# Performance work log

Measured on AMD Instinct MI355X. Metric: run time of the kernel, lower is better.

The kernel has to match this reference:

```python
import jax, jax.numpy as jnp
import numpy as np


def setup_inputs() -> dict:
    key = jax.random.key(0)
    k1, k2, k3 = jax.random.split(key, 3)
    B, D = 4096, 512
    out_ftir = jax.random.normal(k1, (B, D), dtype=jnp.float32)
    out_raman = jax.random.normal(k2, (B, D), dtype=jnp.float32)
    labels = jax.random.randint(k3, (B,), 0, 1000, dtype=jnp.int64)
    # learned parameter: log_tau = log(1/init_tau), init_tau = 0.07
    log_tau = jnp.asarray(np.log(1.0 / 0.07), dtype=jnp.float32)
    return {"out_ftir": out_ftir, "out_raman": out_raman, "labels": labels, "log_tau": log_tau}


def reference(out_ftir, out_raman, labels, log_tau):
    # temperature scale, clamped above at 100
    tau = jnp.minimum(jnp.exp(log_tau), 100.0)
    # [B, B] similarity logits
    logits = (out_ftir @ out_raman.T) * tau
    # CLIP-style symmetric cross-entropy with diagonal targets (arange(B)).
    # Note: original torch code's loop over positive off-diagonal pairs
    # computes an unused tensor and does not affect the output.
    raman_lp = jnp.diagonal(jax.nn.log_softmax(logits, axis=-1))   # rows: ftir -> raman
    ftir_lp = jnp.diagonal(jax.nn.log_softmax(logits.T, axis=-1))  # cols: raman -> ftir
    raman_loss = -jnp.mean(raman_lp)
    ftir_loss = -jnp.mean(ftir_lp)
    return (ftir_loss + raman_loss) / 2.0
```

## Files before the change

kernel.cpp:

```cpp
#include <hip/hip_runtime.h>
#include <hip/hip_bf16.h>
#include <stdint.h>


typedef float f32x4 __attribute__((ext_vector_type(4)));
typedef __bf16 bf16x8 __attribute__((ext_vector_type(8)));
typedef __bf16 bf16x4 __attribute__((ext_vector_type(4)));

#define B_DIM 4096
#define D_DIM 512
#define NCHUNK 32

__device__ __forceinline__ void gld_lds16(const void* g, void* l) {
  __builtin_amdgcn_global_load_lds(
      (const __attribute__((address_space(1))) unsigned int*)g,
      (__attribute__((address_space(3))) unsigned int*)l,
      16, 0, 0);
}

__global__ __launch_bounds__(256) void cast_diag_kernel(
    const float* __restrict__ A, const float* __restrict__ Bm,
    __bf16* __restrict__ Abf, __bf16* __restrict__ Bbf,
    float* __restrict__ diagp, float* __restrict__ acc,
    unsigned* __restrict__ counter) {
  if (blockIdx.x == 0 && threadIdx.x == 0) { acc[0] = 0.f; counter[0] = 0u; }
  const float4* A4 = (const float4*)A;
  const float4* B4 = (const float4*)Bm;
  bf16x4* Ab4 = (bf16x4*)Abf;
  bf16x4* Bb4 = (bf16x4*)Bbf;
  int idx = blockIdx.x * 256 + threadIdx.x;
  float local = 0.f;
  #pragma unroll
  for (int it = 0; it < 4; ++it, idx += 512 * 256) {
    int row = idx >> 7, el4 = idx & 127;
    int swzG = ((el4 >> 1) ^ row) & 7;
    int el4p = (el4 & 0x71) | (swzG << 1);
    int pidx = row * 128 + el4p;
    float4 va = A4[idx], vb = B4[idx];
    bf16x4 oa, ob;
    oa[0] = (__bf16)va.x; oa[1] = (__bf16)va.y; oa[2] = (__bf16)va.z; oa[3] = (__bf16)va.w;
    ob[0] = (__bf16)vb.x; ob[1] = (__bf16)vb.y; ob[2] = (__bf16)vb.z; ob[3] = (__bf16)vb.w;
    Ab4[pidx] = oa; Bb4[pidx] = ob;
    local += va.x*vb.x + va.y*vb.y + va.z*vb.z + va.w*vb.w;
  }
  #pragma unroll
  for (int off = 1; off < 64; off <<= 1) local += __shfl_xor(local, off);
  __shared__ float red[4];
  int w = threadIdx.x >> 6, lane = threadIdx.x & 63;
  if (lane == 0) red[w] = local;
  __syncthreads();
  if (threadIdx.x == 0)
    diagp[blockIdx.x] = red[0] + red[1] + red[2] + red[3];
}

__global__ __launch_bounds__(256) void gemm_lse_kernel(
    const __bf16* __restrict__ A, const __bf16* __restrict__ Bm,
    const float* __restrict__ log_tau,
    float* __restrict__ row_pmax, float* __restrict__ row_psum,
    float* __restrict__ col_pmax, float* __restrict__ col_psum) {
  __shared__ char smem[34816];
  __bf16* Alds = (__bf16*)smem;
  __bf16* Blds = (__bf16*)(smem + 16384);
  const int blk = blockIdx.x;
  const int xcd = blk & 7, local = blk >> 3;
  const int bm = (xcd & 3) * 8 + (local & 7);
  const int bn = (xcd >> 2) * 16 + (local >> 3);
  const int t = threadIdx.x;
  const int lane = t & 63;
  const int w = t >> 6;
  const int wm = (w >> 1) * 64, wn = (w & 1) * 64;
  const int q = lane >> 4, c16 = lane & 15, swz = c16 & 7;

  f32x4 acc[4][4] = {};

  const char* Ag = (const char*)(A + (size_t)(bm * 128 + (t >> 3)) * D_DIM + (t & 7) * 8);
  const char* Bg = (const char*)(Bm + (size_t)(bn * 128 + (t >> 3)) * D_DIM + (t & 7) * 8);
  char* Al = (char*)Alds + t * 16;
  char* Bl = (char*)Blds + t * 16;

  for (int kt = 0; kt < 8; ++kt) {
    const char* ag = Ag + kt * 128;
    const char* bg = Bg + kt * 128;
    #pragma unroll
    for (int i = 0; i < 4; ++i) {
      gld_lds16(ag + i * 32 * 1024, Al + i * 4096);
      gld_lds16(bg + i * 32 * 1024, Bl + i * 4096);
    }
    __syncthreads();
    const __bf16* Abase = Alds + (wm + c16) * 64;
    const __bf16* Bbase = Blds + (wn + c16) * 64;
    #pragma unroll
    for (int h = 0; h < 2; ++h) {
      const int kb = ((h << 2) | q) ^ swz;
      bf16x8 af[4], bfr[4];
      #pragma unroll
      for (int mi = 0; mi < 4; ++mi)
        af[mi] = *(const bf16x8*)(Abase + mi * 1024 + kb * 8);
      #pragma unroll
      for (int ni = 0; ni < 4; ++ni)
        bfr[ni] = *(const bf16x8*)(Bbase + ni * 1024 + kb * 8);
      #pragma unroll
      for (int mi = 0; mi < 4; ++mi)
        #pragma unroll
        for (int ni = 0; ni < 4; ++ni)
          acc[mi][ni] = __builtin_amdgcn_mfma_f32_16x16x32_bf16(af[mi], bfr[ni], acc[mi][ni], 0, 0, 0);
    }
    __syncthreads();
  }

  const float tau = fminf(__expf(log_tau[0]), 100.0f);
  #pragma unroll
  for (int mi = 0; mi < 4; ++mi)
    #pragma unroll
    for (int ni = 0; ni < 4; ++ni)
      acc[mi][ni] *= tau;

  float2* rbuf = (float2*)smem;
  #pragma unroll
  for (int mi = 0; mi < 4; ++mi)
    #pragma unroll
    for (int r = 0; r < 4; ++r) {
      float v0 = acc[mi][0][r], v1 = acc[mi][1][r], v2 = acc[mi][2][r], v3 = acc[mi][3][r];
      float m = fmaxf(fmaxf(v0, v1), fmaxf(v2, v3));
      float s = __expf(v0 - m) + __expf(v1 - m) + __expf(v2 - m) + __expf(v3 - m);
      int R = wm + mi * 16 + q * 4 + r;
      rbuf[R * 33 + (w & 1) * 16 + c16] = make_float2(m, s);
    }
  __syncthreads();
  if (t < 128) {
    float M = rbuf[t * 33].x;
    #pragma unroll
    for (int x = 1; x < 32; ++x) M = fmaxf(M, rbuf[t * 33 + x].x);
    float S = 0.f;
    #pragma unroll
    for (int x = 0; x < 32; ++x) { float2 p = rbuf[t * 33 + x]; S += p.y * __expf(p.x - M); }
    row_pmax[bn * B_DIM + bm * 128 + t] = M;
    row_psum[bn * B_DIM + bm * 128 + t] = S;
  }
  __syncthreads();
  float2* cbuf = (float2*)smem;
  #pragma unroll
  for (int ni = 0; ni < 4; ++ni) {
    float m = -3.0e38f;
    #pragma unroll
    for (int mi = 0; mi < 4; ++mi)
      #pragma unroll
      for (int r = 0; r < 4; ++r) m = fmaxf(m, acc[mi][ni][r]);
    float s = 0.f;
    #pragma unroll
    for (int mi = 0; mi < 4; ++mi)
      #pragma unroll
      for (int r = 0; r < 4; ++r) s += __expf(acc[mi][ni][r] - m);
    int C = wn + ni * 16 + c16;
    cbuf[C * 9 + (w >> 1) * 4 + q] = make_float2(m, s);
  }
  __syncthreads();
  if (t < 128) {
    float M = cbuf[t * 9].x;
    #pragma unroll
    for (int y = 1; y < 8; ++y) M = fmaxf(M, cbuf[t * 9 + y].x);
    float S = 0.f;
    #pragma unroll
    for (int y = 0; y < 8; ++y) { float2 p = cbuf[t * 9 + y]; S += p.y * __expf(p.x - M); }
    col_pmax[bm * B_DIM + bn * 128 + t] = M;
    col_psum[bm * B_DIM + bn * 128 + t] = S;
  }
}

__global__ __launch_bounds__(256) void combine_kernel(
    const float* __restrict__ row_pmax, const float* __restrict__ row_psum,
    const float* __restrict__ col_pmax, const float* __restrict__ col_psum,
    const float* __restrict__ diagp, const float* __restrict__ log_tau,
    float* __restrict__ acc, unsigned* __restrict__ counter,
    float* __restrict__ out) {
  const int t = threadIdx.x;
  const int item = blockIdx.x * 256 + t;
  const float* pm; const float* ps; int i;
  if (item < B_DIM) { pm = row_pmax; ps = row_psum; i = item; }
  else              { pm = col_pmax; ps = col_psum; i = item - B_DIM; }
  float M = pm[i];
  #pragma unroll
  for (int k = 1; k < NCHUNK; ++k) M = fmaxf(M, pm[k * B_DIM + i]);
  float S = 0.f;
  #pragma unroll
  for (int k = 0; k < NCHUNK; ++k) S += ps[k * B_DIM + i] * __expf(pm[k * B_DIM + i] - M);
  float local = M + __logf(S);
  if (blockIdx.x == 0) {
    float tau = fminf(__expf(log_tau[0]), 100.0f);
    local += -2.0f * tau * (diagp[t] + diagp[t + 256]);
  }
  #pragma unroll
  for (int off = 1; off < 64; off <<= 1) local += __shfl_xor(local, off);
  __shared__ float red[4];
  int w = t >> 6, lane = t & 63;
  if (lane == 0) red[w] = local;
  __syncthreads();
  if (t == 0) {
    atomicAdd(acc, red[0] + red[1] + red[2] + red[3]);
    __threadfence();
    unsigned old = atomicAdd(counter, 1u);
    if (old == 31u) {
      float v = atomicAdd(acc, 0.0f);
      out[0] = v * (1.0f / 8192.0f);
    }
  }
}

extern "C" void kernel_launch(void* const* d_in, const int* in_sizes, int n_in,
                              void* d_out, int out_size, void* d_ws, size_t ws_size,
                              hipStream_t stream) {
  const float* ftir    = (const float*)d_in[0];
  const float* raman   = (const float*)d_in[1];
  const float* log_tau = (const float*)d_in[3];
  float* out = (float*)d_out;

  char* ws = (char*)d_ws;
  __bf16* Abf     = (__bf16*)(ws);
  __bf16* Bbf     = (__bf16*)(ws + (4u << 20));
  float* row_pmax = (float*)(ws + (8u << 20));
  float* row_psum = (float*)(ws + (8u << 20) + (512u << 10));
  float* col_pmax = (float*)(ws + (9u << 20));
  float* col_psum = (float*)(ws + (9u << 20) + (512u << 10));
  float* diagp    = (float*)(ws + (10u << 20));
  float* acc      = (float*)(ws + (10u << 20) + 4096);
  unsigned* cnt   = (unsigned*)(ws + (10u << 20) + 4096 + 4);

  cast_diag_kernel<<<512, 256, 0, stream>>>(ftir, raman, Abf, Bbf, diagp, acc, cnt);
  gemm_lse_kernel<<<1024, 256, 0, stream>>>(Abf, Bbf, log_tau,
                                            row_pmax, row_psum, col_pmax, col_psum);
  combine_kernel<<<32, 256, 0, stream>>>(row_pmax, row_psum, col_pmax, col_psum,
                                         diagp, log_tau, acc, cnt, out);
}
```

Measured before the change: 102.8 us.

## Double-buffer LDS tiles to overlap global loads with MFMA compute

The GEMM main loop now uses two LDS buffers. The loads for the next K-tile are issued right after the barrier, while the current tile is consumed by MFMAs. This replaces the old load, sync, compute, sync pattern and removes one barrier per iteration. The cost is LDS use rising to 64KB per block, which cuts how many blocks fit on a CU at once. The compiler may also insert conservative vmcnt waits that limit the overlap.

New measurement: 97.64 us. 5.0% less time.

```diff
diff --git a/kernel.cpp b/kernel.cpp
--- a/kernel.cpp
+++ b/kernel.cpp
@@ -58,13 +58,11 @@
     const float* __restrict__ log_tau,
     float* __restrict__ row_pmax, float* __restrict__ row_psum,
     float* __restrict__ col_pmax, float* __restrict__ col_psum) {
-  __shared__ char smem[34816];
-  __bf16* Alds = (__bf16*)smem;
-  __bf16* Blds = (__bf16*)(smem + 16384);
+  __shared__ char smem[65536];
   const int blk = blockIdx.x;
-  const int xcd = blk & 7, local = blk >> 3;
-  const int bm = (xcd & 3) * 8 + (local & 7);
-  const int bn = (xcd >> 2) * 16 + (local >> 3);
+  const int xcd = blk & 7, loc = blk >> 3;
+  const int bm = (xcd & 3) * 8 + (loc & 7);
+  const int bn = (xcd >> 2) * 16 + (loc >> 3);
   const int t = threadIdx.x;
   const int lane = t & 63;
   const int w = t >> 6;
@@ -73,22 +71,28 @@
 
   f32x4 acc[4][4] = {};
 
-  const char* Ag = (const char*)(A + (size_t)(bm * 128 + (t >> 3)) * D_DIM + (t & 7) * 8);
-  const char* Bg = (const char*)(Bm + (size_t)(bn * 128 + (t >> 3)) * D_DIM + (t & 7) * 8);
-  char* Al = (char*)Alds + t * 16;
-  char* Bl = (char*)Blds + t * 16;
-
+  const char* Ag = (const char*)A + (size_t)(bm * 128 + (t >> 3)) * 1024 + (t & 7) * 16;
+  const char* Bg = (const char*)Bm + (size_t)(bn * 128 + (t >> 3)) * 1024 + (t & 7) * 16;
+
+  #define ISSUE_STAGE(kt, p)                                                  \
+    do {                                                                      \
+      const char* ag = Ag + (kt) * 128;                                       \
+      const char* bg = Bg + (kt) * 128;                                       \
+      char* Al = smem + (p) * 32768 + t * 16;                                 \
+      char* Bl = smem + (p) * 32768 + 16384 + t * 16;                         \
+      _Pragma("unroll")                                                       \
+      for (int i = 0; i < 4; ++i) {                                           \
+        gld_lds16(ag + i * 32768, Al + i * 4096);                             \
+        gld_lds16(bg + i * 32768, Bl + i * 4096);                             \
+      }                                                                       \
+    } while (0)
+
+  ISSUE_STAGE(0, 0);
   for (int kt = 0; kt < 8; ++kt) {
-    const char* ag = Ag + kt * 128;
-    const char* bg = Bg + kt * 128;
-    #pragma unroll
-    for (int i = 0; i < 4; ++i) {
-      gld_lds16(ag + i * 32 * 1024, Al + i * 4096);
-      gld_lds16(bg + i * 32 * 1024, Bl + i * 4096);
-    }
     __syncthreads();
-    const __bf16* Abase = Alds + (wm + c16) * 64;
-    const __bf16* Bbase = Blds + (wn + c16) * 64;
+    if (kt < 7) ISSUE_STAGE(kt + 1, (kt + 1) & 1);
+    const __bf16* Abase = (const __bf16*)(smem + (kt & 1) * 32768) + (wm + c16) * 64;
+    const __bf16* Bbase = (const __bf16*)(smem + (kt & 1) * 32768 + 16384) + (wn + c16) * 64;
     #pragma unroll
     for (int h = 0; h < 2; ++h) {
       const int kb = ((h << 2) | q) ^ swz;
@@ -105,8 +109,9 @@
         for (int ni = 0; ni < 4; ++ni)
           acc[mi][ni] = __builtin_amdgcn_mfma_f32_16x16x32_bf16(af[mi], bfr[ni], acc[mi][ni], 0, 0, 0);
     }
-    __syncthreads();
-  }
+  }
+  __syncthreads();
+  #undef ISSUE_STAGE
 
   const float tau = fminf(__expf(log_tau[0]), 100.0f);
   #pragma unroll
```
